# Kernel tuning notes

Measured on AMD Instinct MI355X. Metric: run time of the kernel, lower is better.

Reference implementation:

```python
import jax, jax.numpy as jnp
import numpy as np

N = 50000   # num_nodes
E = 800000  # edges for relation 0
DIN = 512
DOUT = 128


def setup_inputs() -> dict:
    key = jax.random.key(0)
    k1, k2, k3 = jax.random.split(key, 3)
    x = jax.random.normal(k1, (N, DIN), dtype=jnp.float32)
    edge_index = jax.random.randint(k2, (2, E), 0, N, dtype=jnp.int64)
    # GCNConv weight (glorot-ish) and zero bias, as after reset_parameters()
    W = jax.random.normal(k3, (DIN, DOUT), dtype=jnp.float32) * (1.0 / np.sqrt(DIN))
    b = jnp.zeros((DOUT,), dtype=jnp.float32)
    return {"x": x, "edge_index": edge_index, "W": W, "b": b,
            "dropout_probability": 0.5}


def _dropout(h, key, p):
    keep = jax.random.bernoulli(key, 1.0 - p, h.shape)
    return jnp.where(keep, h / (1.0 - p), jnp.zeros((), h.dtype))


def _gcn_conv(h, edge_index, W, b):
    # PyG GCNConv: add self-loops, symmetric normalization, XW then scatter-add.
    src, dst = edge_index[0], edge_index[1]
    loops = jnp.arange(N, dtype=src.dtype)
    col = jnp.concatenate([src, loops])  # gather side (source)
    row = jnp.concatenate([dst, loops])  # scatter side (target)
    ones = jnp.ones(row.shape[0], dtype=h.dtype)
    deg = jax.ops.segment_sum(ones, row, num_segments=N)        # in-degree + 1
    dinv = jnp.where(deg > 0, jax.lax.rsqrt(deg), jnp.zeros((), h.dtype))
    norm = dinv[row] * dinv[col]                                # [E+N]
    hw = h @ W                                                  # [N, DOUT] dense GEMM
    msg = hw[col] * norm[:, None]                               # gather + scale
    out = jax.ops.segment_sum(msg, row, num_segments=N)         # scatter-add
    return out + b


def reference(x, edge_index, W, b, dropout_probability):
    # Forward loop in the source breaks after the first relation, so exactly one
    # conv is applied. training=True dropout with fixed keys for determinism.
    p = dropout_probability
    k1, k2, k3 = jax.random.split(jax.random.key(1), 3)

    pos_seq = _dropout(x, k1, p)
    pos_h = jax.nn.relu(_gcn_conv(pos_seq, edge_index, W, b))
    summary = jax.nn.sigmoid(jnp.mean(pos_h, axis=0, keepdims=True))

    neg_seq = _dropout(x, k2, p)
    perm = jax.random.permutation(k3, N)   # torch.randperm corruption
    neg_h = jax.nn.relu(_gcn_conv(neg_seq[perm], edge_index, W, b))

    return (pos_h, neg_h, summary, pos_seq, neg_seq)
```

## Files before the change

kernel.cpp:

```cpp
#include <hip/hip_runtime.h>
#include <stdint.h>

static constexpr int    N_NODES = 50000;
static constexpr int    N_EDGES = 800000;
static constexpr int    DIN     = 512;
static constexpr int    DOUT    = 128;
static constexpr size_t SEQ_ELEMS = (size_t)N_NODES * DIN;
static constexpr size_t H_ELEMS   = (size_t)N_NODES * DOUT;

static constexpr int RS_NB = 49;
static constexpr int EDGE_BLOCKS = 782;
static_assert(N_NODES % 8 == 0, "gather grid assumes 8 nodes/block exactly");

typedef __attribute__((ext_vector_type(8))) short bf16x8;
typedef __attribute__((ext_vector_type(4))) float f32x4;
typedef __attribute__((ext_vector_type(4))) unsigned short u16x4;

static constexpr size_t W_HDR    = 0;
static constexpr size_t W_DEGCNT = 16;
static constexpr size_t W_CURSOR = 50016;
static constexpr size_t W_SUMBUF = 100016;
static constexpr size_t W_CNT    = 100144;
static constexpr size_t W_ZEND   = 100152;
static constexpr size_t W_HIST   = 100152;
static constexpr size_t W_OFFS   = 150328;
static constexpr size_t W_ROWPTR = 175416;
static constexpr size_t W_COLSRC = 225420;
static constexpr size_t W_DINV   = 1025420;
static constexpr size_t W_KEYS   = 1075420;
static constexpr size_t W_VALS   = 1275420;
static constexpr size_t W_RANK   = 1475420;
static constexpr size_t W_PERM   = 1575420;
static constexpr size_t W_BT     = 1625420;
static constexpr size_t W_HWPOS  = 1658188;
static constexpr size_t W_HWNEG  = 4858188;

__device__ __forceinline__ uint16_t f2bf(float f) {
  uint32_t u = __float_as_uint(f);
  return (uint16_t)((u + 0x7FFFu + ((u >> 16) & 1u)) >> 16);
}
__device__ __forceinline__ float b2f(uint16_t h) {
  return __uint_as_float(((uint32_t)h) << 16);
}
__device__ __forceinline__ uint32_t rotl32(uint32_t x, int r) {
  return (x << r) | (x >> (32 - r));
}

__device__ __forceinline__ void threefry2x32(uint32_t k0, uint32_t k1,
                                             uint32_t x0, uint32_t x1,
                                             uint32_t& o0, uint32_t& o1) {
  uint32_t ks0 = k0, ks1 = k1, ks2 = k0 ^ k1 ^ 0x1BD11BDAu;
  x0 += ks0; x1 += ks1;
#define TF_ROUND(r) { x0 += x1; x1 = rotl32(x1, (r)); x1 ^= x0; }
  TF_ROUND(13) TF_ROUND(15) TF_ROUND(26) TF_ROUND(6)
  x0 += ks1; x1 += ks2 + 1u;
  TF_ROUND(17) TF_ROUND(29) TF_ROUND(16) TF_ROUND(24)
  x0 += ks2; x1 += ks0 + 2u;
  TF_ROUND(13) TF_ROUND(15) TF_ROUND(26) TF_ROUND(6)
  x0 += ks0; x1 += ks1 + 3u;
  TF_ROUND(17) TF_ROUND(29) TF_ROUND(16) TF_ROUND(24)
  x0 += ks1; x1 += ks2 + 4u;
  TF_ROUND(13) TF_ROUND(15) TF_ROUND(26) TF_ROUND(6)
  x0 += ks2; x1 += ks0 + 5u;
#undef TF_ROUND
  o0 = x0; o1 = x1;
}

__device__ __forceinline__ uint32_t randbits32(uint32_t k0, uint32_t k1, uint32_t ctr) {
  uint32_t a, b;
  threefry2x32(k0, k1, 0u, ctr, a, b);
  return a ^ b;
}

__global__ void __launch_bounds__(256) wt_init_kernel(const float* __restrict__ W,
                                                      uint32_t* __restrict__ wsu) {
  {
    int gid = blockIdx.x * 256 + threadIdx.x;
    for (size_t i = W_DEGCNT + gid; i < W_ZEND; i += 4096) wsu[i] = 0u;
  }
  if (blockIdx.x == 0 && threadIdx.x == 0) {
    uint32_t k3a, k3b, ra, rb, s1a, s1b, s2a, s2b;
    threefry2x32(0u, 1u, 0u, 2u, k3a, k3b);
    threefry2x32(k3a, k3b, 0u, 0u, ra, rb);
    threefry2x32(k3a, k3b, 0u, 1u, s1a, s1b);
    threefry2x32(ra, rb, 0u, 1u, s2a, s2b);
    wsu[4] = s1a; wsu[5] = s1b; wsu[6] = s2a; wsu[7] = s2b;
  }
  uint16_t* BT = (uint16_t*)(wsu + W_BT);
  __shared__ float tile[32][129];
  int k0 = blockIdx.x * 32;
  int t = threadIdx.x;
  for (int i = t; i < 32 * 128; i += 256) {
    int k = i >> 7, n = i & 127;
    tile[k][n] = W[(size_t)(k0 + k) * DOUT + n];
  }
  __syncthreads();
  for (int i = t; i < 32 * 128; i += 256) {
    int n = i >> 5, k = i & 31;
    BT[(size_t)n * DIN + k0 + k] = f2bf(tile[k][n]);
  }
}

__global__ void __launch_bounds__(1024) fusedA_kernel(const int* __restrict__ ei,
                                                      uint32_t* __restrict__ wsu) {
  int b = blockIdx.x;
  if (b < EDGE_BLOCKS) {
    int e = b * 1024 + threadIdx.x;
    if (e < N_EDGES) atomicAdd(&wsu[W_DEGCNT + ei[N_EDGES + e]], 1u);
  } else {
    __shared__ uint32_t h[256];
    int sb = b - EDGE_BLOCKS, s = sb / RS_NB, bb = sb % RS_NB;
    int t = threadIdx.x;
    if (t < 256) h[t] = 0u;
    __syncthreads();
    uint32_t k0 = wsu[4 + 2 * s], k1 = wsu[5 + 2 * s];
    int p = bb * 1024 + t;
    if (p < N_NODES) {
      uint32_t kv = randbits32(k0, k1, (uint32_t)p);
      wsu[W_KEYS + (size_t)s * 100000 + p] = kv;
      wsu[W_VALS + (size_t)s * 100000 + p] = (uint32_t)p;
      atomicAdd(&h[kv & 255u], 1u);
    }
    __syncthreads();
    if (t < 256) wsu[W_HIST + (size_t)s * 25088 + t * RS_NB + bb] = h[t];
  }
}

__device__ __forceinline__ void scan12544(const uint32_t* __restrict__ hist,
                                          uint32_t* __restrict__ offs,
                                          uint32_t* __restrict__ zeroT,
                                          uint32_t* __restrict__ sc) {
  const int t = threadIdx.x;
  int c0 = t * 13, c1 = c0 + 13;
  if (c0 > 12544) c0 = 12544;
  if (c1 > 12544) c1 = 12544;
  uint32_t loc[13];
  uint32_t sum = 0;
  for (int c = c0; c < c1; ++c) {
    uint32_t v = hist[c];
    loc[c - c0] = v;
    sum += v;
  }
  sc[t] = sum;
  __syncthreads();
  for (int off = 1; off < 1024; off <<= 1) {
    uint32_t xx = (t >= off) ? sc[t - off] : 0u;
    __syncthreads();
    sc[t] += xx;
    __syncthreads();
  }
  uint32_t run = sc[t] - sum;
  for (int c = c0; c < c1; ++c) {
    offs[c] = run;
    run += loc[c - c0];
  }
  if (zeroT != nullptr)
    for (int i = t; i < 12544; i += 1024) zeroT[i] = 0u;
}

__global__ void __launch_bounds__(1024) fusedB_kernel(uint32_t* __restrict__ wsu) {
  __shared__ uint32_t sc[1024];
  int b = blockIdx.x, t = threadIdx.x;
  if (b == 0) {
    int c0 = t * 49, c1 = c0 + 49;
    if (c0 > N_NODES) c0 = N_NODES;
    if (c1 > N_NODES) c1 = N_NODES;
    float* dinv = (float*)(wsu + W_DINV);
    uint32_t sum = 0;
    for (int c = c0; c < c1; ++c) {
      uint32_t v = wsu[W_DEGCNT + c];
      dinv[c] = __frsqrt_rn((float)(v + 1u));
      sum += v;
    }
    sc[t] = sum;
    __syncthreads();
    for (int off = 1; off < 1024; off <<= 1) {
      uint32_t xx = (t >= off) ? sc[t - off] : 0u;
      __syncthreads();
      sc[t] += xx;
      __syncthreads();
    }
    uint32_t run = sc[t] - sum;
    for (int c = c0; c < c1; ++c) {
      uint32_t h = wsu[W_DEGCNT + c];
      wsu[W_ROWPTR + c] = run;
      run += h;
    }
    if (t == 0) wsu[W_ROWPTR + N_NODES] = (uint32_t)N_EDGES;
  } else {
    int s = b - 1;
    scan12544(wsu + W_HIST + (size_t)s * 25088, wsu + W_OFFS + (size_t)s * 12544,
              wsu + W_HIST + (size_t)s * 25088 + 12544, sc);
  }
}

__global__ void __launch_bounds__(1024) fill_kernel(const int* __restrict__ ei,
                                                    uint32_t* __restrict__ wsu) {
  int e = blockIdx.x * 1024 + threadIdx.x;
  if (e < N_EDGES) {
    int src = ei[e], dst = ei[N_EDGES + e];
    uint32_t pos = wsu[W_ROWPTR + dst] + atomicAdd(&wsu[W_CURSOR + dst], 1u);
    wsu[W_COLSRC + pos] = (uint32_t)src;
  }
}

template <int PASS>
__global__ void __launch_bounds__(1024) scat_kernel(uint32_t* __restrict__ wsu) {
  __shared__ uint32_t gh[4096];
  const int b = blockIdx.x;
  const int s = b / RS_NB, bb = b % RS_NB;
  const int t = threadIdx.x;
  constexpr int shift = PASS * 8;
  const uint32_t* ki = wsu + W_KEYS + (size_t)s * 100000 + (PASS & 1) * 50000;
  const uint32_t* vi = wsu + W_VALS + (size_t)s * 100000 + (PASS & 1) * 50000;
  uint32_t* ko = wsu + W_KEYS + (size_t)s * 100000 + ((PASS + 1) & 1) * 50000;
  uint32_t* vo = wsu + W_VALS + (size_t)s * 100000 + ((PASS + 1) & 1) * 50000;
  const uint32_t* offs = wsu + W_OFFS + (size_t)s * 12544;
  uint32_t* histN = wsu + W_HIST + (size_t)s * 25088 + ((PASS + 1) & 1) * 12544;
  uint32_t* rank = wsu + W_RANK + (size_t)s * 50000;

  for (int i = t; i < 4096; i += 1024) gh[i] = 0u;
  __syncthreads();
  const int w = t >> 6, l = t & 63;
  const uint64_t pre = (1ull << l) - 1ull;
  int p = bb * 1024 + t;
  bool valid = p < N_NODES;
  uint32_t kv = valid ? ki[p] : 0u;
  uint32_t d = (kv >> shift) & 255u;
  uint64_t m = __ballot(valid);
#pragma unroll
  for (int bit = 0; bit < 8; ++bit) {
    uint64_t bbm = __ballot((d >> bit) & 1u);
    m &= ((d >> bit) & 1u) ? bbm : ~bbm;
  }
  int peer = __popcll(m & pre);
  if (valid && peer == 0) gh[w * 256 + d] = (uint32_t)__popcll(m);
  __syncthreads();
  if (t < 256) {
    uint32_t run = 0;
#pragma unroll
    for (int g = 0; g < 16; ++g) {
      uint32_t tmp = gh[g * 256 + t];
      gh[g * 256 + t] = run;
      run += tmp;
    }
  }
  __syncthreads();
  if (valid) {
    uint32_t pos = offs[d * RS_NB + bb] + gh[w * 256 + d] + (uint32_t)peer;
    uint32_t pv = vi[p];
    if constexpr (PASS == 3) {
      if (pv < (uint32_t)N_NODES && pos < (uint32_t)N_NODES)
        rank[pv] = pos;
    } else {
      if (pos < (uint32_t)N_NODES) {
        ko[pos] = kv;
        vo[pos] = pv;
        atomicAdd(&histN[((kv >> (shift + 8)) & 255u) * RS_NB + (pos >> 10)], 1u);
      }
    }
  }
}

template <int PASS>
__global__ void __launch_bounds__(1024) scan_kernel(uint32_t* __restrict__ wsu) {
  __shared__ uint32_t sc[1024];
  int s = blockIdx.x;
  const uint32_t* h = wsu + W_HIST + (size_t)s * 25088 + (PASS & 1) * 12544;
  uint32_t* of = wsu + W_OFFS + (size_t)s * 12544;
  uint32_t* z = (PASS < 3) ? (wsu + W_HIST + (size_t)s * 25088 + ((PASS + 1) & 1) * 12544)
                           : nullptr;
  scan12544(h, of, z, sc);
}

__global__ void __launch_bounds__(1024) invperm_kernel(uint32_t* __restrict__ wsu) {
  int j = blockIdx.x * 1024 + threadIdx.x;
  if (j < N_NODES) {
    uint32_t r1 = wsu[W_RANK + j];
    uint32_t r2 = (r1 < (uint32_t)N_NODES) ? wsu[W_RANK + 50000 + r1] : 0u;
    wsu[W_PERM + j] = (r2 < (uint32_t)N_NODES) ? r2 : 0u;
  }
}

__global__ void __launch_bounds__(256) dg_kernel(const float* __restrict__ x,
                                                 const uint16_t* __restrict__ BT,
                                                 const float* __restrict__ pprob,
                                                 const float* __restrict__ dinv,
                                                 const uint32_t* __restrict__ invp,
                                                 float* __restrict__ seq_pos,
                                                 float* __restrict__ seq_neg,
                                                 uint16_t* __restrict__ hw_pos,
                                                 uint16_t* __restrict__ hw_neg, int M) {
  __shared__ __align__(16) uint16_t ldsA[64 * 64];
  __shared__ __align__(16) uint16_t ldsB[128 * 64];
  const int which = blockIdx.y;
  float*    seq = which ? seq_neg : seq_pos;
  uint16_t* hwb = which ? hw_neg : hw_pos;

  uint32_t kk0, kk1;
  threefry2x32(0u, 1u, 0u, (uint32_t)which, kk0, kk1);
  const float p = pprob[0];
  const float keep_p = 1.0f - p;
  const float scale  = 1.0f / keep_p;
  uint32_t Tint = (uint32_t)ceilf(keep_p * 8388608.0f);
  uint32_t Tu = (Tint >= (1u << 23)) ? 0xFFFFFFFFu : (Tint << 9);

  const int tid  = threadIdx.x;
  const int lane = tid & 63;
  const int w    = tid >> 6;
  const int wr   = w >> 1, wc = w & 1;
  const int m0   = blockIdx.x * 64;
  const int l15  = lane & 15, l4 = lane >> 4;
  const int lr   = lane >> 3, lk = (lane & 7) * 8;

  f32x4 acc[2][4] = {};

  for (int k0 = 0; k0 < DIN; k0 += 64) {
#pragma unroll
    for (int s = 0; s < 4; ++s) {
      int nbase = w * 32 + s * 8;
      const uint16_t* gp = BT + (size_t)(nbase + lr) * DIN + k0 + lk;
      __builtin_amdgcn_global_load_lds(
          (const __attribute__((address_space(1))) void*)gp,
          (__attribute__((address_space(3))) void*)(ldsB + nbase * 64), 16, 0, 0);
    }
    __builtin_amdgcn_sched_barrier(0);
#pragma unroll
    for (int i = 0; i < 4; ++i) {
      int idx = tid + i * 256;
      int row = idx >> 4, q = idx & 15;
      int grow = m0 + row;
      int crow = (grow < M) ? grow : (M - 1);
      float4 v = *reinterpret_cast<const float4*>(x + (size_t)crow * DIN + k0 + q * 4);
      float r[4] = {v.x, v.y, v.z, v.w};
      uint32_t cbase = (uint32_t)crow * DIN + k0 + q * 4;
#pragma unroll
      for (int j = 0; j < 4; ++j) {
        uint32_t bits = randbits32(kk0, kk1, cbase + j);
        r[j] = (bits < Tu) ? r[j] * scale : 0.0f;
      }
      *reinterpret_cast<float4*>(seq + (size_t)crow * DIN + k0 + q * 4) =
          make_float4(r[0], r[1], r[2], r[3]);
      uint32_t u0 = __float_as_uint(r[0]), u1 = __float_as_uint(r[1]);
      uint32_t lo = (u0 >> 16) | (u1 & 0xFFFF0000u);
      u0 = __float_as_uint(r[2]); u1 = __float_as_uint(r[3]);
      uint32_t hi = (u0 >> 16) | (u1 & 0xFFFF0000u);
      *reinterpret_cast<uint2*>(&ldsA[row * 64 + q * 4]) = make_uint2(lo, hi);
    }
    asm volatile("s_waitcnt vmcnt(4) lgkmcnt(0)" ::: "memory");
    __builtin_amdgcn_s_barrier();
    __builtin_amdgcn_sched_barrier(0);
#pragma unroll
    for (int kk = 0; kk < 2; ++kk) {
      bf16x8 afr[2], bfr[4];
#pragma unroll
      for (int f = 0; f < 2; ++f)
        afr[f] = *reinterpret_cast<const bf16x8*>(ldsA + (wr * 32 + f * 16 + l15) * 64 + kk * 32 + l4 * 8);
#pragma unroll
      for (int f = 0; f < 4; ++f)
        bfr[f] = *reinterpret_cast<const bf16x8*>(ldsB + (wc * 64 + f * 16 + l15) * 64 + kk * 32 + l4 * 8);
#pragma unroll
      for (int fm = 0; fm < 2; ++fm)
#pragma unroll
        for (int fn = 0; fn < 4; ++fn)
          acc[fm][fn] = __builtin_amdgcn_mfma_f32_16x16x32_bf16(afr[fm], bfr[fn], acc[fm][fn], 0, 0, 0);
    }
    __builtin_amdgcn_s_barrier();
  }
#pragma unroll
  for (int fm = 0; fm < 2; ++fm) {
#pragma unroll
    for (int r = 0; r < 4; ++r) {
      int row = m0 + wr * 32 + fm * 16 + l4 * 4 + r;
      if (row < M) {
        uint32_t slot = which ? invp[row] : (uint32_t)row;
        float sc = dinv[slot];
        uint16_t* cp = hwb + (size_t)slot * DOUT + wc * 64 + l15;
#pragma unroll
        for (int fn = 0; fn < 4; ++fn)
          cp[fn * 16] = f2bf(acc[fm][fn][r] * sc);
      }
    }
  }
}

__global__ void __launch_bounds__(256) gcn_gather_kernel(const uint16_t* __restrict__ hwP,
                                                         const uint16_t* __restrict__ hwN,
                                                         const float* __restrict__ dinv,
                                                         const uint32_t* __restrict__ rowptr,
                                                         const uint32_t* __restrict__ colsrc,
                                                         const float* __restrict__ bias,
                                                         float* __restrict__ out_pos,
                                                         float* __restrict__ out_neg) {
  int node = blockIdx.x * 8 + (threadIdx.x >> 5);
  int c4 = (threadIdx.x & 31) * 4;
  uint32_t e0 = rowptr[node], e1 = rowptr[node + 1];
  float px = 0.f, py = 0.f, pz = 0.f, pw = 0.f;
  float nx = 0.f, ny = 0.f, nz = 0.f, nw = 0.f;
  uint32_t e = e0;
  for (; e + 4 <= e1; e += 4) {
    uint32_t s0 = colsrc[e], s1 = colsrc[e + 1], s2 = colsrc[e + 2], s3 = colsrc[e + 3];
    u16x4 p0 = *reinterpret_cast<const u16x4*>(hwP + (size_t)s0 * DOUT + c4);
    u16x4 p1 = *reinterpret_cast<const u16x4*>(hwP + (size_t)s1 * DOUT + c4);
    u16x4 p2 = *reinterpret_cast<const u16x4*>(hwP + (size_t)s2 * DOUT + c4);
    u16x4 p3 = *reinterpret_cast<const u16x4*>(hwP + (size_t)s3 * DOUT + c4);
    u16x4 n0 = *reinterpret_cast<const u16x4*>(hwN + (size_t)s0 * DOUT + c4);
    u16x4 n1 = *reinterpret_cast<const u16x4*>(hwN + (size_t)s1 * DOUT + c4);
    u16x4 n2 = *reinterpret_cast<const u16x4*>(hwN + (size_t)s2 * DOUT + c4);
    u16x4 n3 = *reinterpret_cast<const u16x4*>(hwN + (size_t)s3 * DOUT + c4);
    px += (b2f(p0.x) + b2f(p1.x)) + (b2f(p2.x) + b2f(p3.x));
    py += (b2f(p0.y) + b2f(p1.y)) + (b2f(p2.y) + b2f(p3.y));
    pz += (b2f(p0.z) + b2f(p1.z)) + (b2f(p2.z) + b2f(p3.z));
    pw += (b2f(p0.w) + b2f(p1.w)) + (b2f(p2.w) + b2f(p3.w));
    nx += (b2f(n0.x) + b2f(n1.x)) + (b2f(n2.x) + b2f(n3.x));
    ny += (b2f(n0.y) + b2f(n1.y)) + (b2f(n2.y) + b2f(n3.y));
    nz += (b2f(n0.z) + b2f(n1.z)) + (b2f(n2.z) + b2f(n3.z));
    nw += (b2f(n0.w) + b2f(n1.w)) + (b2f(n2.w) + b2f(n3.w));
  }
  for (; e < e1; ++e) {
    uint32_t s = colsrc[e];
    u16x4 vp = *reinterpret_cast<const u16x4*>(hwP + (size_t)s * DOUT + c4);
    u16x4 vn = *reinterpret_cast<const u16x4*>(hwN + (size_t)s * DOUT + c4);
    px += b2f(vp.x); py += b2f(vp.y); pz += b2f(vp.z); pw += b2f(vp.w);
    nx += b2f(vn.x); ny += b2f(vn.y); nz += b2f(vn.z); nw += b2f(vn.w);
  }
  u16x4 sp = *reinterpret_cast<const u16x4*>(hwP + (size_t)node * DOUT + c4);
  u16x4 sn = *reinterpret_cast<const u16x4*>(hwN + (size_t)node * DOUT + c4);
  float4 bv = *reinterpret_cast<const float4*>(bias + c4);
  float dn = dinv[node];
  float4 op, on;
  op.x = fmaxf(dn * (px + b2f(sp.x)) + bv.x, 0.0f);
  op.y = fmaxf(dn * (py + b2f(sp.y)) + bv.y, 0.0f);
  op.z = fmaxf(dn * (pz + b2f(sp.z)) + bv.z, 0.0f);
  op.w = fmaxf(dn * (pw + b2f(sp.w)) + bv.w, 0.0f);
  on.x = fmaxf(dn * (nx + b2f(sn.x)) + bv.x, 0.0f);
  on.y = fmaxf(dn * (ny + b2f(sn.y)) + bv.y, 0.0f);
  on.z = fmaxf(dn * (nz + b2f(sn.z)) + bv.z, 0.0f);
  on.w = fmaxf(dn * (nw + b2f(sn.w)) + bv.w, 0.0f);
  *reinterpret_cast<float4*>(out_pos + (size_t)node * DOUT + c4) = op;
  *reinterpret_cast<float4*>(out_neg + (size_t)node * DOUT + c4) = on;
}

__global__ void __launch_bounds__(128) colsum_sig_kernel(const float* __restrict__ ph,
                                                         float* __restrict__ sumbuf,
                                                         uint32_t* __restrict__ counter,
                                                         float* __restrict__ outs) {
  int c = threadIdx.x;
  int r0 = blockIdx.x * 256;
  int r1 = r0 + 256; if (r1 > N_NODES) r1 = N_NODES;
  float s = 0.0f;
  for (int r = r0; r < r1; ++r) s += ph[(size_t)r * DOUT + c];
  atomicAdd(&sumbuf[c], s);
  __threadfence();
  __syncthreads();
  __shared__ uint32_t lastflag;
  if (c == 0) lastflag = atomicAdd(counter, 1u);
  __syncthreads();
  if (lastflag == gridDim.x - 1) {
    __threadfence();
    float m = atomicAdd(&sumbuf[c], 0.0f) * (1.0f / (float)N_NODES);
    outs[c] = 1.0f / (1.0f + expf(-m));
  }
}

extern "C" void kernel_launch(void* const* d_in, const int* in_sizes, int n_in,
                              void* d_out, int out_size, void* d_ws, size_t ws_size,
                              hipStream_t stream) {
  const float* x     = (const float*)d_in[0];
  const int*   ei    = (const int*)d_in[1];
  const float* W     = (const float*)d_in[2];
  const float* bias  = (const float*)d_in[3];
  const float* pprob = (const float*)d_in[4];

  float* out = (float*)d_out;
  float* out_pos_h   = out;
  float* out_neg_h   = out + H_ELEMS;
  float* out_summary = out + 2 * H_ELEMS;
  float* out_pos_seq = out + 2 * H_ELEMS + DOUT;
  float* out_neg_seq = out_pos_seq + SEQ_ELEMS;

  uint32_t* wsu    = (uint32_t*)d_ws;
  float*    sumbuf = (float*)(wsu + W_SUMBUF);
  uint32_t* rowptr = wsu + W_ROWPTR;
  uint32_t* colsrc = wsu + W_COLSRC;
  float*    dinv   = (float*)(wsu + W_DINV);
  uint32_t* invp   = wsu + W_PERM;
  uint16_t* BT     = (uint16_t*)(wsu + W_BT);
  uint16_t* hw_pos = (uint16_t*)(wsu + W_HWPOS);
  uint16_t* hw_neg = (uint16_t*)(wsu + W_HWNEG);

  wt_init_kernel<<<DIN / 32, 256, 0, stream>>>(W, wsu);

  fusedA_kernel<<<EDGE_BLOCKS + 2 * RS_NB, 1024, 0, stream>>>(ei, wsu);

  fusedB_kernel<<<3, 1024, 0, stream>>>(wsu);

  fill_kernel<<<EDGE_BLOCKS, 1024, 0, stream>>>(ei, wsu);

  scat_kernel<0><<<2 * RS_NB, 1024, 0, stream>>>(wsu);
  scan_kernel<1><<<2, 1024, 0, stream>>>(wsu);
  scat_kernel<1><<<2 * RS_NB, 1024, 0, stream>>>(wsu);
  scan_kernel<2><<<2, 1024, 0, stream>>>(wsu);
  scat_kernel<2><<<2 * RS_NB, 1024, 0, stream>>>(wsu);
  scan_kernel<3><<<2, 1024, 0, stream>>>(wsu);
  scat_kernel<3><<<2 * RS_NB, 1024, 0, stream>>>(wsu);

  invperm_kernel<<<RS_NB, 1024, 0, stream>>>(wsu);

  dim3 dgrid((N_NODES + 63) / 64, 2);
  dg_kernel<<<dgrid, 256, 0, stream>>>(x, BT, pprob, dinv, invp,
                                       out_pos_seq, out_neg_seq, hw_pos, hw_neg, N_NODES);

  gcn_gather_kernel<<<N_NODES / 8, 256, 0, stream>>>(hw_pos, hw_neg, dinv, rowptr,
                                                     colsrc, bias, out_pos_h, out_neg_h);

  colsum_sig_kernel<<<(N_NODES + 255) / 256, 128, 0, stream>>>(out_pos_h, sumbuf,
                                                               wsu + W_CNT + 3, out_summary);

  (void)in_sizes; (void)n_in; (void)out_size; (void)ws_size;
}
```

Measured before the change: 575.9 us.

## Interleave pos/neg HW rows, fuse CSR fill with first radix pass, inline inverse perm

Stores the positive and negative XW results in one interleaved bf16 buffer (256 values per node), so the gather kernel does one 16-byte load per edge per lane covering both branches instead of two 8-byte loads from separate arrays. The CSR fill kernel is merged with the first radix scatter pass into one launch, and the inverse-permutation kernel is removed by doing the two-level rank lookup inside the GEMM epilogue. Together these cut kernel launches and make the random-access gathers wider. In exchange the epilogue does an extra dependent load, and the edge loop is unrolled by 8, which raises register pressure.

```diff
diff --git a/kernel.cpp b/kernel.cpp
--- a/kernel.cpp
+++ b/kernel.cpp
@@ -15,6 +15,7 @@
 typedef __attribute__((ext_vector_type(8))) short bf16x8;
 typedef __attribute__((ext_vector_type(4))) float f32x4;
 typedef __attribute__((ext_vector_type(4))) unsigned short u16x4;
+typedef __attribute__((ext_vector_type(8))) unsigned short u16x8;
 
 static constexpr size_t W_HDR    = 0;
 static constexpr size_t W_DEGCNT = 16;
@@ -30,10 +31,8 @@
 static constexpr size_t W_KEYS   = 1075420;
 static constexpr size_t W_VALS   = 1275420;
 static constexpr size_t W_RANK   = 1475420;
-static constexpr size_t W_PERM   = 1575420;
 static constexpr size_t W_BT     = 1625420;
-static constexpr size_t W_HWPOS  = 1658188;
-static constexpr size_t W_HWNEG  = 4858188;
+static constexpr size_t W_HWI    = 1658188;
 
 __device__ __forceinline__ uint16_t f2bf(float f) {
   uint32_t u = __float_as_uint(f);
@@ -194,21 +193,9 @@
   }
 }
 
-__global__ void __launch_bounds__(1024) fill_kernel(const int* __restrict__ ei,
-                                                    uint32_t* __restrict__ wsu) {
-  int e = blockIdx.x * 1024 + threadIdx.x;
-  if (e < N_EDGES) {
-    int src = ei[e], dst = ei[N_EDGES + e];
-    uint32_t pos = wsu[W_ROWPTR + dst] + atomicAdd(&wsu[W_CURSOR + dst], 1u);
-    wsu[W_COLSRC + pos] = (uint32_t)src;
-  }
-}
-
 template <int PASS>
-__global__ void __launch_bounds__(1024) scat_kernel(uint32_t* __restrict__ wsu) {
-  __shared__ uint32_t gh[4096];
-  const int b = blockIdx.x;
-  const int s = b / RS_NB, bb = b % RS_NB;
+__device__ __forceinline__ void scatter_body(int s, int bb, uint32_t* __restrict__ wsu,
+                                             uint32_t* __restrict__ gh) {
   const int t = threadIdx.x;
   constexpr int shift = PASS * 8;
   const uint32_t* ki = wsu + W_KEYS + (size_t)s * 100000 + (PASS & 1) * 50000;
@@ -262,6 +249,30 @@
   }
 }
 
+__global__ void __launch_bounds__(1024) fusedC_kernel(const int* __restrict__ ei,
+                                                      uint32_t* __restrict__ wsu) {
+  __shared__ uint32_t gh[4096];
+  int b = blockIdx.x;
+  if (b < EDGE_BLOCKS) {
+    int e = b * 1024 + threadIdx.x;
+    if (e < N_EDGES) {
+      int src = ei[e], dst = ei[N_EDGES + e];
+      uint32_t pos = wsu[W_ROWPTR + dst] + atomicAdd(&wsu[W_CURSOR + dst], 1u);
+      wsu[W_COLSRC + pos] = (uint32_t)src;
+    }
+  } else {
+    int sb = b - EDGE_BLOCKS;
+    scatter_body<0>(sb / RS_NB, sb % RS_NB, wsu, gh);
+  }
+}
+
+template <int PASS>
+__global__ void __launch_bounds__(1024) scat_kernel(uint32_t* __restrict__ wsu) {
+  __shared__ uint32_t gh[4096];
+  int b = blockIdx.x;
+  scatter_body<PASS>(b / RS_NB, b % RS_NB, wsu, gh);
+}
+
 template <int PASS>
 __global__ void __launch_bounds__(1024) scan_kernel(uint32_t* __restrict__ wsu) {
   __shared__ uint32_t sc[1024];
@@ -273,29 +284,19 @@
   scan12544(h, of, z, sc);
 }
 
-__global__ void __launch_bounds__(1024) invperm_kernel(uint32_t* __restrict__ wsu) {
-  int j = blockIdx.x * 1024 + threadIdx.x;
-  if (j < N_NODES) {
-    uint32_t r1 = wsu[W_RANK + j];
-    uint32_t r2 = (r1 < (uint32_t)N_NODES) ? wsu[W_RANK + 50000 + r1] : 0u;
-    wsu[W_PERM + j] = (r2 < (uint32_t)N_NODES) ? r2 : 0u;
-  }
-}
-
 __global__ void __launch_bounds__(256) dg_kernel(const float* __restrict__ x,
                                                  const uint16_t* __restrict__ BT,
                                                  const float* __restrict__ pprob,
                                                  const float* __restrict__ dinv,
-                                                 const uint32_t* __restrict__ invp,
+                                                 const uint32_t* __restrict__ rankA,
+                                                 const uint32_t* __restrict__ rankB,
                                                  float* __restrict__ seq_pos,
                                                  float* __restrict__ seq_neg,
-                                                 uint16_t* __restrict__ hw_pos,
-                                                 uint16_t* __restrict__ hw_neg, int M) {
+                                                 uint16_t* __restrict__ hwI, int M) {
   __shared__ __align__(16) uint16_t ldsA[64 * 64];
   __shared__ __align__(16) uint16_t ldsB[128 * 64];
   const int which = blockIdx.y;
-  float*    seq = which ? seq_neg : seq_pos;
-  uint16_t* hwb = which ? hw_neg : hw_pos;
+  float* seq = which ? seq_neg : seq_pos;
 
   uint32_t kk0, kk1;
   threefry2x32(0u, 1u, 0u, (uint32_t)which, kk0, kk1);
@@ -373,9 +374,14 @@
     for (int r = 0; r < 4; ++r) {
       int row = m0 + wr * 32 + fm * 16 + l4 * 4 + r;
       if (row < M) {
-        uint32_t slot = which ? invp[row] : (uint32_t)row;
+        uint32_t slot = (uint32_t)row;
+        if (which) {
+          uint32_t r1 = rankA[row];
+          slot = (r1 < (uint32_t)N_NODES) ? rankB[r1] : 0u;
+          if (slot >= (uint32_t)N_NODES) slot = 0u;
+        }
         float sc = dinv[slot];
-        uint16_t* cp = hwb + (size_t)slot * DOUT + wc * 64 + l15;
+        uint16_t* cp = hwI + (size_t)slot * 256 + which * 128 + wc * 64 + l15;
 #pragma unroll
         for (int fn = 0; fn < 4; ++fn)
           cp[fn * 16] = f2bf(acc[fm][fn][r] * sc);
@@ -384,61 +390,57 @@
   }
 }
 
-__global__ void __launch_bounds__(256) gcn_gather_kernel(const uint16_t* __restrict__ hwP,
-                                                         const uint16_t* __restrict__ hwN,
+__global__ void __launch_bounds__(256) gcn_gather_kernel(const uint16_t* __restrict__ hwI,
                                                          const float* __restrict__ dinv,
                                                          const uint32_t* __restrict__ rowptr,
                                                          const uint32_t* __restrict__ colsrc,
                                                          const float* __restrict__ bias,
                                                          float* __restrict__ out_pos,
                                                          float* __restrict__ out_neg) {
-  int node = blockIdx.x * 8 + (threadIdx.x >> 5);
-  int c4 = (threadIdx.x & 31) * 4;
+  const int t = threadIdx.x;
+  int node = blockIdx.x * 8 + (t >> 5);
+  int lane32 = t & 31;
+  int c8 = (lane32 & 15) * 8;
+  int half = lane32 >> 4;
   uint32_t e0 = rowptr[node], e1 = rowptr[node + 1];
-  float px = 0.f, py = 0.f, pz = 0.f, pw = 0.f;
-  float nx = 0.f, ny = 0.f, nz = 0.f, nw = 0.f;
+  float a0 = 0.f, a1 = 0.f, a2 = 0.f, a3 = 0.f, a4 = 0.f, a5 = 0.f, a6 = 0.f, a7 = 0.f;
   uint32_t e = e0;
-  for (; e + 4 <= e1; e += 4) {
-    uint32_t s0 = colsrc[e], s1 = colsrc[e + 1], s2 = colsrc[e + 2], s3 = colsrc[e + 3];
-    u16x4 p0 = *reinterpret_cast<const u16x4*>(hwP + (size_t)s0 * DOUT + c4);
-    u16x4 p1 = *reinterpret_cast<const u16x4*>(hwP + (size_t)s1 * DOUT + c4);
-    u16x4 p2 = *reinterpret_cast<const u16x4*>(hwP + (size_t)s2 * DOUT + c4);
-    u16x4 p3 = *reinterpret_cast<const u16x4*>(hwP + (size_t)s3 * DOUT + c4);
-    u16x4 n0 = *reinterpret_cast<const u16x4*>(hwN + (size_t)s0 * DOUT + c4);
-    u16x4 n1 = *reinterpret_cast<const u16x4*>(hwN + (size_t)s1 * DOUT + c4);
-    u16x4 n2 = *reinterpret_cast<const u16x4*>(hwN + (size_t)s2 * DOUT + c4);
-    u16x4 n3 = *reinterpret_cast<const u16x4*>(hwN + (size_t)s3 * DOUT + c4);
-    px += (b2f(p0.x) + b2f(p1.x)) + (b2f(p2.x) + b2f(p3.x));
-    py += (b2f(p0.y) + b2f(p1.y)) + (b2f(p2.y) + b2f(p3.y));
-    pz += (b2f(p0.z) + b2f(p1.z)) + (b2f(p2.z) + b2f(p3.z));
-    pw += (b2f(p0.w) + b2f(p1.w)) + (b2f(p2.w) + b2f(p3.w));
-    nx += (b2f(n0.x) + b2f(n1.x)) + (b2f(n2.x) + b2f(n3.x));
-    ny += (b2f(n0.y) + b2f(n1.y)) + (b2f(n2.y) + b2f(n3.y));
-    nz += (b2f(n0.z) + b2f(n1.z)) + (b2f(n2.z) + b2f(n3.z));
-    nw += (b2f(n0.w) + b2f(n1.w)) + (b2f(n2.w) + b2f(n3.w));
+  for (; e + 8 <= e1; e += 8) {
+    uint32_t ss[8];
+#pragma unroll
+    for (int j = 0; j < 8; ++j) ss[j] = colsrc[e + j];
+    u16x8 vv[8];
+#pragma unroll
+    for (int j = 0; j < 8; ++j)
+      vv[j] = *reinterpret_cast<const u16x8*>(hwI + (size_t)ss[j] * 256 + lane32 * 8);
+#pragma unroll
+    for (int j = 0; j < 8; ++j) {
+      a0 += b2f(vv[j][0]); a1 += b2f(vv[j][1]); a2 += b2f(vv[j][2]); a3 += b2f(vv[j][3]);
+      a4 += b2f(vv[j][4]); a5 += b2f(vv[j][5]); a6 += b2f(vv[j][6]); a7 += b2f(vv[j][7]);
+    }
   }
   for (; e < e1; ++e) {
     uint32_t s = colsrc[e];
-    u16x4 vp = *reinterpret_cast<const u16x4*>(hwP + (size_t)s * DOUT + c4);
-    u16x4 vn = *reinterpret_cast<const u16x4*>(hwN + (size_t)s * DOUT + c4);
-    px += b2f(vp.x); py += b2f(vp.y); pz += b2f(vp.z); pw += b2f(vp.w);
-    nx += b2f(vn.x); ny += b2f(vn.y); nz += b2f(vn.z); nw += b2f(vn.w);
-  }
-  u16x4 sp = *reinterpret_cast<const u16x4*>(hwP + (size_t)node * DOUT + c4);
-  u16x4 sn = *reinterpret_cast<const u16x4*>(hwN + (size_t)node * DOUT + c4);
-  float4 bv = *reinterpret_cast<const float4*>(bias + c4);
+    u16x8 v = *reinterpret_cast<const u16x8*>(hwI + (size_t)s * 256 + lane32 * 8);
+    a0 += b2f(v[0]); a1 += b2f(v[1]); a2 += b2f(v[2]); a3 += b2f(v[3]);
+    a4 += b2f(v[4]); a5 += b2f(v[5]); a6 += b2f(v[6]); a7 += b2f(v[7]);
+  }
+  u16x8 sv = *reinterpret_cast<const u16x8*>(hwI + (size_t)node * 256 + lane32 * 8);
   float dn = dinv[node];
-  float4 op, on;
-  op.x = fmaxf(dn * (px + b2f(sp.x)) + bv.x, 0.0f);
-  op.y = fmaxf(dn * (py + b2f(sp.y)) + bv.y, 0.0f);
-  op.z = fmaxf(dn * (pz + b2f(sp.z)) + bv.z, 0.0f);
-  op.w = fmaxf(dn * (pw + b2f(sp.w)) + bv.w, 0.0f);
-  on.x = fmaxf(dn * (nx + b2f(sn.x)) + bv.x, 0.0f);
-  on.y = fmaxf(dn * (ny + b2f(sn.y)) + bv.y, 0.0f);
-  on.z = fmaxf(dn * (nz + b2f(sn.z)) + bv.z, 0.0f);
-  on.w = fmaxf(dn * (nw + b2f(sn.w)) + bv.w, 0.0f);
-  *reinterpret_cast<float4*>(out_pos + (size_t)node * DOUT + c4) = op;
-  *reinterpret_cast<float4*>(out_neg + (size_t)node * DOUT + c4) = on;
+  float4 b0 = *reinterpret_cast<const float4*>(bias + c8);
+  float4 b1 = *reinterpret_cast<const float4*>(bias + c8 + 4);
+  float4 o0, o1;
+  o0.x = fmaxf(dn * (a0 + b2f(sv[0])) + b0.x, 0.0f);
+  o0.y = fmaxf(dn * (a1 + b2f(sv[1])) + b0.y, 0.0f);
+  o0.z = fmaxf(dn * (a2 + b2f(sv[2])) + b0.z, 0.0f);
+  o0.w = fmaxf(dn * (a3 + b2f(sv[3])) + b0.w, 0.0f);
+  o1.x = fmaxf(dn * (a4 + b2f(sv[4])) + b1.x, 0.0f);
+  o1.y = fmaxf(dn * (a5 + b2f(sv[5])) + b1.y, 0.0f);
+  o1.z = fmaxf(dn * (a6 + b2f(sv[6])) + b1.z, 0.0f);
+  o1.w = fmaxf(dn * (a7 + b2f(sv[7])) + b1.w, 0.0f);
+  float* dst = (half ? out_neg : out_pos) + (size_t)node * DOUT + c8;
+  *reinterpret_cast<float4*>(dst)     = o0;
+  *reinterpret_cast<float4*>(dst + 4) = o1;
 }
 
 __global__ void __launch_bounds__(128) colsum_sig_kernel(const float* __restrict__ ph,
@@ -484,10 +486,10 @@
   uint32_t* rowptr = wsu + W_ROWPTR;
   uint32_t* colsrc = wsu + W_COLSRC;
   float*    dinv   = (float*)(wsu + W_DINV);
-  uint32_t* invp   = wsu + W_PERM;
+  uint32_t* rankA  = wsu + W_RANK;
+  uint32_t* rankB  = wsu + W_RANK + 50000;
   uint16_t* BT     = (uint16_t*)(wsu + W_BT);
-  uint16_t* hw_pos = (uint16_t*)(wsu + W_HWPOS);
-  uint16_t* hw_neg = (uint16_t*)(wsu + W_HWNEG);
+  uint16_t* hwI    = (uint16_t*)(wsu + W_HWI);
 
   wt_init_kernel<<<DIN / 32, 256, 0, stream>>>(W, wsu);
 
@@ -495,9 +497,8 @@
 
   fusedB_kernel<<<3, 1024, 0, stream>>>(wsu);
 
-  fill_kernel<<<EDGE_BLOCKS, 1024, 0, stream>>>(ei, wsu);
-
-  scat_kernel<0><<<2 * RS_NB, 1024, 0, stream>>>(wsu);
+  fusedC_kernel<<<EDGE_BLOCKS + 2 * RS_NB, 1024, 0, stream>>>(ei, wsu);
+
   scan_kernel<1><<<2, 1024, 0, stream>>>(wsu);
   scat_kernel<1><<<2 * RS_NB, 1024, 0, stream>>>(wsu);
   scan_kernel<2><<<2, 1024, 0, stream>>>(wsu);
@@ -505,14 +506,12 @@
   scan_kernel<3><<<2, 1024, 0, stream>>>(wsu);
   scat_kernel<3><<<2 * RS_NB, 1024, 0, stream>>>(wsu);
 
-  invperm_kernel<<<RS_NB, 1024, 0, stream>>>(wsu);
-
   dim3 dgrid((N_NODES + 63) / 64, 2);
-  dg_kernel<<<dgrid, 256, 0, stream>>>(x, BT, pprob, dinv, invp,
-                                       out_pos_seq, out_neg_seq, hw_pos, hw_neg, N_NODES);
-
-  gcn_gather_kernel<<<N_NODES / 8, 256, 0, stream>>>(hw_pos, hw_neg, dinv, rowptr,
-                                                     colsrc, bias, out_pos_h, out_neg_h);
+  dg_kernel<<<dgrid, 256, 0, stream>>>(x, BT, pprob, dinv, rankA, rankB,
+                                       out_pos_seq, out_neg_seq, hwI, N_NODES);
+
+  gcn_gather_kernel<<<N_NODES / 8, 256, 0, stream>>>(hwI, dinv, rowptr, colsrc,
+                                                     bias, out_pos_h, out_neg_h);
 
   colsum_sig_kernel<<<(N_NODES + 255) / 256, 128, 0, stream>>>(out_pos_h, sumbuf,
                                                                wsu + W_CNT + 3, out_summary);
```

Result: faster. 554.9 us (-3.6%).
